# Kernel tuning notes

Measured on AMD Instinct MI355X. Metric: run time of the kernel, lower is better.

## Reference

```python
import jax, jax.numpy as jnp
import numpy as np

B, IN_F, K_INT, OUT_F = 256, 512, 75, 64
INIT = 0.05


def setup_inputs() -> dict:
    key = jax.random.key(0)
    k_x, k_t = jax.random.split(key)
    x = jax.random.normal(k_x, (B, IN_F), dtype=jnp.float32)
    T = jax.random.normal(k_t, (IN_F, K_INT, OUT_F), dtype=jnp.float32) * INIT
    return {"x": x, "T": T}


def reference(x, T):
    # M: [B, K, O] = x @ T flattened over (K, O)
    Bn = x.shape[0]
    M = (x @ T.reshape(T.shape[0], -1)).reshape(Bn, T.shape[1], T.shape[2])
    # pairwise L1 distance over K: [B, B, O]
    # (original materializes [B, B, K, O] broadcasted diff; same math)
    M_diff = M[None, :, :, :] - M[:, None, :, :]
    distance = jnp.abs(M_diff).sum(axis=2)           # [B, B, O]
    exp_distance = jnp.exp(-distance)                # [B, B, O]
    minibatch_features = exp_distance.sum(axis=1) - 1.0  # [B, O]; -1 removes self-distance
    return minibatch_features
```

## Files before the change

kernel.cpp:

```cpp
#include <hip/hip_runtime.h>


typedef __attribute__((ext_vector_type(8))) short bf16x8;
typedef __attribute__((ext_vector_type(4))) float f32x4;
typedef unsigned short u16;
typedef unsigned int u32;

__device__ inline u16 f2bf(float f) {
  u32 u = __float_as_uint(f);
  return (u16)((u + 0x7FFFu + ((u >> 16) & 1u)) >> 16);
}

__global__ __launch_bounds__(256) void cvt_x(const float* __restrict__ x,
                                             u16* __restrict__ xb) {
  const int i = blockIdx.x * 256 + threadIdx.x;
  const float4* x4 = reinterpret_cast<const float4*>(x);
  const float4 v0 = x4[i * 2], v1 = x4[i * 2 + 1];
  uint4 o;
  o.x = (u32)f2bf(v0.x) | ((u32)f2bf(v0.y) << 16);
  o.y = (u32)f2bf(v0.z) | ((u32)f2bf(v0.w) << 16);
  o.z = (u32)f2bf(v1.x) | ((u32)f2bf(v1.y) << 16);
  o.w = (u32)f2bf(v1.z) | ((u32)f2bf(v1.w) << 16);
  *reinterpret_cast<uint4*>(xb + i * 8) = o;
}

__global__ __launch_bounds__(256) void cvt_T(const float* __restrict__ T,
                                             u16* __restrict__ Tb) {
  const int f0 = blockIdx.x << 6;
  const int k = blockIdx.y;
  const int tid = threadIdx.x;
  __shared__ float tile[64][65];

  const float4* T4 = reinterpret_cast<const float4*>(T);
  const int r = tid >> 2;
  const int c = tid & 3;
#pragma unroll
  for (int h = 0; h < 4; ++h) {
    const int q = c + (h << 2);
    const float4 v = T4[(f0 + r) * 1200 + k * 16 + q];
    tile[r][(q << 2) + 0] = v.x;
    tile[r][(q << 2) + 1] = v.y;
    tile[r][(q << 2) + 2] = v.z;
    tile[r][(q << 2) + 3] = v.w;
  }
  __syncthreads();

  const int w = tid >> 2;
  u16 us[16];
#pragma unroll
  for (int j = 0; j < 16; ++j) us[j] = f2bf(tile[(c << 4) + j][w]);
  uint4 p0, p1;
  p0.x = (u32)us[0] | ((u32)us[1] << 16);
  p0.y = (u32)us[2] | ((u32)us[3] << 16);
  p0.z = (u32)us[4] | ((u32)us[5] << 16);
  p0.w = (u32)us[6] | ((u32)us[7] << 16);
  p1.x = (u32)us[8] | ((u32)us[9] << 16);
  p1.y = (u32)us[10] | ((u32)us[11] << 16);
  p1.z = (u32)us[12] | ((u32)us[13] << 16);
  p1.w = (u32)us[14] | ((u32)us[15] << 16);
  uint4* dst = reinterpret_cast<uint4*>(Tb + ((k << 6) + w) * 512 + f0 + (c << 4));
  dst[0] = p0;
  dst[1] = p1;
}

__global__ __launch_bounds__(256) void md_gemm_mfma(const u16* __restrict__ Tb,
                                                    const u16* __restrict__ xb,
                                                    float* __restrict__ Mt) {
  const int tid = threadIdx.x;
  const int l = tid & 63, w = tid >> 6;
  const int n0 = (blockIdx.x << 6) + ((w >> 1) << 5);
  const int b0 = (blockIdx.y << 6) + ((w & 1) << 5);
  const int lr = l & 15;
  const int ko = (l >> 4) << 3;

  const u16* pa0 = Tb + (n0 + lr) * 512 + ko;
  const u16* pa1 = pa0 + 16 * 512;
  const u16* pb0 = xb + (b0 + lr) * 512 + ko;
  const u16* pb1 = pb0 + 16 * 512;

  f32x4 d00 = {0.f, 0.f, 0.f, 0.f}, d01 = d00, d10 = d00, d11 = d00;

#pragma unroll 4
  for (int kk = 0; kk < 16; ++kk) {
    const int off = kk << 5;
    const bf16x8 a0 = *reinterpret_cast<const bf16x8*>(pa0 + off);
    const bf16x8 a1 = *reinterpret_cast<const bf16x8*>(pa1 + off);
    const bf16x8 f0 = *reinterpret_cast<const bf16x8*>(pb0 + off);
    const bf16x8 f1 = *reinterpret_cast<const bf16x8*>(pb1 + off);
    d00 = __builtin_amdgcn_mfma_f32_16x16x32_bf16(a0, f0, d00, 0, 0, 0);
    d01 = __builtin_amdgcn_mfma_f32_16x16x32_bf16(a0, f1, d01, 0, 0, 0);
    d10 = __builtin_amdgcn_mfma_f32_16x16x32_bf16(a1, f0, d10, 0, 0, 0);
    d11 = __builtin_amdgcn_mfma_f32_16x16x32_bf16(a1, f1, d11, 0, 0, 0);
  }

#pragma unroll
  for (int r = 0; r < 4; ++r) {
    const int row = ((l >> 4) << 2) + r;
    {
      const int n = n0 + row;
      float* base = Mt + (n & 63) * 19200 + (n >> 6) * 256;
      base[b0 + lr] = d00[r];
      base[b0 + 16 + lr] = d01[r];
    }
    {
      const int n = n0 + 16 + row;
      float* base = Mt + (n & 63) * 19200 + (n >> 6) * 256;
      base[b0 + lr] = d10[r];
      base[b0 + 16 + lr] = d11[r];
    }
  }
}

__global__ __launch_bounds__(256) void md_pair_sym(const float* __restrict__ Mt,
                                                   float* __restrict__ ps) {
  const int bid = blockIdx.x;
  const int o = bid & 63;
  const int tp = bid >> 6;
  const int TI[10] = {0, 0, 0, 0, 1, 1, 1, 2, 2, 3};
  const int TJ[10] = {0, 1, 2, 3, 1, 2, 3, 2, 3, 3};
  const int ti = TI[tp], tj = TJ[tp];
  const int tid = threadIdx.x;
  const bool diag = (ti == tj);

  __shared__ alignas(16) float sm[2 * 75 * 64];
  float4* Mi4 = reinterpret_cast<float4*>(sm);
  float4* Mj4 = diag ? Mi4 : Mi4 + 75 * 16;

  {
    const float4* src = reinterpret_cast<const float4*>(Mt + o * 19200 + ti * 64);
    for (int t = tid; t < 1200; t += 256) {
      const int k = t >> 4, q = t & 15;
      Mi4[k * 16 + q] = src[k * 64 + q];
    }
    if (!diag) {
      const float4* srj = reinterpret_cast<const float4*>(Mt + o * 19200 + tj * 64);
      for (int t = tid; t < 1200; t += 256) {
        const int k = t >> 4, q = t & 15;
        Mj4[k * 16 + q] = srj[k * 64 + q];
      }
    }
  }
  __syncthreads();

  const int io = tid & 15;
  const int js = tid >> 4;

  float d[4][4];
#pragma unroll
  for (int a = 0; a < 4; ++a)
#pragma unroll
    for (int b = 0; b < 4; ++b) d[a][b] = 0.0f;

  for (int k = 0; k < 75; ++k) {
    const float4 vi = Mi4[k * 16 + io];
    const float4 vj = Mj4[k * 16 + js];
    const float via[4] = {vi.x, vi.y, vi.z, vi.w};
    const float vja[4] = {vj.x, vj.y, vj.z, vj.w};
#pragma unroll
    for (int a = 0; a < 4; ++a)
#pragma unroll
      for (int b = 0; b < 4; ++b) d[a][b] += __builtin_fabsf(vja[b] - via[a]);
  }

  float isum[4] = {0.f, 0.f, 0.f, 0.f};
  float jsum[4] = {0.f, 0.f, 0.f, 0.f};
#pragma unroll
  for (int a = 0; a < 4; ++a)
#pragma unroll
    for (int b = 0; b < 4; ++b) {
      const float e = __expf(-d[a][b]);
      isum[a] += e;
      jsum[b] += e;
    }

  __syncthreads();
  float* red = sm;
#pragma unroll
  for (int a = 0; a < 4; ++a) red[((io << 2) + a) * 17 + js] = isum[a];
  __syncthreads();
  if (tid < 64) {
    float s = 0.0f;
#pragma unroll
    for (int c = 0; c < 16; ++c) s += red[tid * 17 + c];
    ps[(((o << 2) + ti) << 2 | tj) * 64 + tid] = s;
  }
  if (!diag) {
    __syncthreads();
#pragma unroll
    for (int b = 0; b < 4; ++b) red[((js << 2) + b) * 17 + io] = jsum[b];
    __syncthreads();
    if (tid < 64) {
      float s = 0.0f;
#pragma unroll
      for (int c = 0; c < 16; ++c) s += red[tid * 17 + c];
      ps[(((o << 2) + tj) << 2 | ti) * 64 + tid] = s;
    }
  }
}

__global__ __launch_bounds__(256) void md_reduce(const float* __restrict__ ps,
                                                 float* __restrict__ out) {
  const int idx = blockIdx.x * 256 + threadIdx.x;
  const int i = idx >> 6, o = idx & 63;
  const int g = i >> 6, il = i & 63;
  float s = 0.0f;
#pragma unroll
  for (int c = 0; c < 4; ++c) s += ps[(((o << 2) + g) << 2 | c) * 64 + il];
  out[i * 64 + o] = s - 1.0f;
}

extern "C" void kernel_launch(void* const* d_in, const int* in_sizes, int n_in,
                              void* d_out, int out_size, void* d_ws, size_t ws_size,
                              hipStream_t stream) {
  const float* x = (const float*)d_in[0];
  const float* T = (const float*)d_in[1];
  float* out = (float*)d_out;

  char* ws = (char*)d_ws;
  float* Mt = (float*)ws;
  u16* Tb = (u16*)(ws + 4915200);
  u16* xb = (u16*)(ws + 9830400);
  float* ps = (float*)(ws + 10092544);

  cvt_x<<<64, 256, 0, stream>>>(x, xb);
  cvt_T<<<dim3(8, 75), 256, 0, stream>>>(T, Tb);
  md_gemm_mfma<<<dim3(75, 4), 256, 0, stream>>>(Tb, xb, Mt);
  md_pair_sym<<<640, 256, 0, stream>>>(Mt, ps);
  md_reduce<<<64, 256, 0, stream>>>(ps, out);
}
```

Baseline: 53.24 us.

## Merge conversion kernels and replace symmetric pair tiles with full 64-row blocks

Folds the x and T bf16 conversion kernels into one launch. Replaces the symmetric 10-tile pair kernel plus separate reduce kernel with a kernel where each block loads all 256 samples for one output feature and computes 64 rows times 256 columns directly. Each thread now holds an 8x8 register tile and reduces with wave shuffles, writing the final output directly. This removes two launches and the partial-sum buffer, but gives up the symmetry saving, so pairwise work roughly doubles, and the 8x8 tile raises register pressure with only 256 blocks.

Measured after the change: 58.39 us. +9.7%, slower.

```diff
diff --git a/kernel.cpp b/kernel.cpp
--- a/kernel.cpp
+++ b/kernel.cpp
@@ -11,24 +11,28 @@
   return (u16)((u + 0x7FFFu + ((u >> 16) & 1u)) >> 16);
 }
 
-__global__ __launch_bounds__(256) void cvt_x(const float* __restrict__ x,
-                                             u16* __restrict__ xb) {
-  const int i = blockIdx.x * 256 + threadIdx.x;
-  const float4* x4 = reinterpret_cast<const float4*>(x);
-  const float4 v0 = x4[i * 2], v1 = x4[i * 2 + 1];
-  uint4 o;
-  o.x = (u32)f2bf(v0.x) | ((u32)f2bf(v0.y) << 16);
-  o.y = (u32)f2bf(v0.z) | ((u32)f2bf(v0.w) << 16);
-  o.z = (u32)f2bf(v1.x) | ((u32)f2bf(v1.y) << 16);
-  o.w = (u32)f2bf(v1.z) | ((u32)f2bf(v1.w) << 16);
-  *reinterpret_cast<uint4*>(xb + i * 8) = o;
-}
-
-__global__ __launch_bounds__(256) void cvt_T(const float* __restrict__ T,
-                                             u16* __restrict__ Tb) {
-  const int f0 = blockIdx.x << 6;
-  const int k = blockIdx.y;
+__global__ __launch_bounds__(256) void cvt_all(const float* __restrict__ x,
+                                               const float* __restrict__ T,
+                                               u16* __restrict__ xb,
+                                               u16* __restrict__ Tb) {
+  const int bid = blockIdx.x;
   const int tid = threadIdx.x;
+
+  if (bid >= 600) {
+    const int i = (bid - 600) * 256 + tid;
+    const float4* x4 = reinterpret_cast<const float4*>(x);
+    const float4 v0 = x4[i * 2], v1 = x4[i * 2 + 1];
+    uint4 o;
+    o.x = (u32)f2bf(v0.x) | ((u32)f2bf(v0.y) << 16);
+    o.y = (u32)f2bf(v0.z) | ((u32)f2bf(v0.w) << 16);
+    o.z = (u32)f2bf(v1.x) | ((u32)f2bf(v1.y) << 16);
+    o.w = (u32)f2bf(v1.z) | ((u32)f2bf(v1.w) << 16);
+    *reinterpret_cast<uint4*>(xb + i * 8) = o;
+    return;
+  }
+
+  const int f0 = (bid & 7) << 6;
+  const int k = bid >> 3;
   __shared__ float tile[64][65];
 
   const float4* T4 = reinterpret_cast<const float4*>(T);
@@ -111,102 +115,73 @@
   }
 }
 
-__global__ __launch_bounds__(256) void md_pair_sym(const float* __restrict__ Mt,
-                                                   float* __restrict__ ps) {
+__global__ __launch_bounds__(256, 1) void md_pair2(const float* __restrict__ Mt,
+                                                   float* __restrict__ out) {
   const int bid = blockIdx.x;
   const int o = bid & 63;
-  const int tp = bid >> 6;
-  const int TI[10] = {0, 0, 0, 0, 1, 1, 1, 2, 2, 3};
-  const int TJ[10] = {0, 1, 2, 3, 1, 2, 3, 2, 3, 3};
-  const int ti = TI[tp], tj = TJ[tp];
+  const int ibase = (bid >> 6) << 6;
   const int tid = threadIdx.x;
-  const bool diag = (ti == tj);
-
-  __shared__ alignas(16) float sm[2 * 75 * 64];
-  float4* Mi4 = reinterpret_cast<float4*>(sm);
-  float4* Mj4 = diag ? Mi4 : Mi4 + 75 * 16;
+
+  __shared__ alignas(16) float Ms[75 * 256];
 
   {
-    const float4* src = reinterpret_cast<const float4*>(Mt + o * 19200 + ti * 64);
-    for (int t = tid; t < 1200; t += 256) {
-      const int k = t >> 4, q = t & 15;
-      Mi4[k * 16 + q] = src[k * 64 + q];
-    }
-    if (!diag) {
-      const float4* srj = reinterpret_cast<const float4*>(Mt + o * 19200 + tj * 64);
-      for (int t = tid; t < 1200; t += 256) {
-        const int k = t >> 4, q = t & 15;
-        Mj4[k * 16 + q] = srj[k * 64 + q];
-      }
-    }
-  }
-  __syncthreads();
-
-  const int io = tid & 15;
-  const int js = tid >> 4;
-
-  float d[4][4];
-#pragma unroll
-  for (int a = 0; a < 4; ++a)
-#pragma unroll
-    for (int b = 0; b < 4; ++b) d[a][b] = 0.0f;
-
+    const float4* src = reinterpret_cast<const float4*>(Mt + o * 19200);
+    float4* dst = reinterpret_cast<float4*>(Ms);
+    for (int t = tid; t < 4800; t += 256) dst[t] = src[t];
+  }
+  __syncthreads();
+
+  const int is = tid & 7;
+  const int js = tid >> 3;
+  const int ifq = ((ibase >> 2) + (is << 1));
+
+  float d[8][8];
+#pragma unroll
+  for (int a = 0; a < 8; ++a)
+#pragma unroll
+    for (int b = 0; b < 8; ++b) d[a][b] = 0.0f;
+
+#pragma unroll 2
   for (int k = 0; k < 75; ++k) {
-    const float4 vi = Mi4[k * 16 + io];
-    const float4 vj = Mj4[k * 16 + js];
-    const float via[4] = {vi.x, vi.y, vi.z, vi.w};
-    const float vja[4] = {vj.x, vj.y, vj.z, vj.w};
-#pragma unroll
-    for (int a = 0; a < 4; ++a)
-#pragma unroll
-      for (int b = 0; b < 4; ++b) d[a][b] += __builtin_fabsf(vja[b] - via[a]);
-  }
-
-  float isum[4] = {0.f, 0.f, 0.f, 0.f};
-  float jsum[4] = {0.f, 0.f, 0.f, 0.f};
-#pragma unroll
-  for (int a = 0; a < 4; ++a)
-#pragma unroll
-    for (int b = 0; b < 4; ++b) {
-      const float e = __expf(-d[a][b]);
-      isum[a] += e;
-      jsum[b] += e;
-    }
-
-  __syncthreads();
-  float* red = sm;
-#pragma unroll
-  for (int a = 0; a < 4; ++a) red[((io << 2) + a) * 17 + js] = isum[a];
+    const float4* row4 = reinterpret_cast<const float4*>(Ms + (k << 8));
+    const float4 vi0 = row4[ifq];
+    const float4 vi1 = row4[ifq + 1];
+    const float4 vj0 = row4[(js << 1)];
+    const float4 vj1 = row4[(js << 1) + 1];
+    const float ia[8] = {vi0.x, vi0.y, vi0.z, vi0.w, vi1.x, vi1.y, vi1.z, vi1.w};
+    const float ja[8] = {vj0.x, vj0.y, vj0.z, vj0.w, vj1.x, vj1.y, vj1.z, vj1.w};
+#pragma unroll
+    for (int a = 0; a < 8; ++a)
+#pragma unroll
+      for (int b = 0; b < 8; ++b) d[a][b] += __builtin_fabsf(ja[b] - ia[a]);
+  }
+
+  float isum[8];
+#pragma unroll
+  for (int a = 0; a < 8; ++a) {
+    float s = 0.0f;
+#pragma unroll
+    for (int b = 0; b < 8; ++b) s += __expf(-d[a][b]);
+    isum[a] = s;
+  }
+
+#pragma unroll
+  for (int m = 8; m <= 32; m <<= 1)
+#pragma unroll
+    for (int a = 0; a < 8; ++a) isum[a] += __shfl_xor(isum[a], m);
+
+  __syncthreads();
+  float* red = Ms;
+  const int wv = tid >> 6;
+  if (((tid >> 3) & 7) == 0) {
+#pragma unroll
+    for (int a = 0; a < 8; ++a) red[wv * 72 + (is << 3) + a] = isum[a];
+  }
   __syncthreads();
   if (tid < 64) {
-    float s = 0.0f;
-#pragma unroll
-    for (int c = 0; c < 16; ++c) s += red[tid * 17 + c];
-    ps[(((o << 2) + ti) << 2 | tj) * 64 + tid] = s;
-  }
-  if (!diag) {
-    __syncthreads();
-#pragma unroll
-    for (int b = 0; b < 4; ++b) red[((js << 2) + b) * 17 + io] = jsum[b];
-    __syncthreads();
-    if (tid < 64) {
-      float s = 0.0f;
-#pragma unroll
-      for (int c = 0; c < 16; ++c) s += red[tid * 17 + c];
-      ps[(((o << 2) + tj) << 2 | ti) * 64 + tid] = s;
-    }
-  }
-}
-
-__global__ __launch_bounds__(256) void md_reduce(const float* __restrict__ ps,
-                                                 float* __restrict__ out) {
-  const int idx = blockIdx.x * 256 + threadIdx.x;
-  const int i = idx >> 6, o = idx & 63;
-  const int g = i >> 6, il = i & 63;
-  float s = 0.0f;
-#pragma unroll
-  for (int c = 0; c < 4; ++c) s += ps[(((o << 2) + g) << 2 | c) * 64 + il];
-  out[i * 64 + o] = s - 1.0f;
+    const float s = red[tid] + red[72 + tid] + red[144 + tid] + red[216 + tid];
+    out[(ibase + tid) * 64 + o] = s - 1.0f;
+  }
 }
 
 extern "C" void kernel_launch(void* const* d_in, const int* in_sizes, int n_in,
@@ -220,11 +195,8 @@
   float* Mt = (float*)ws;
   u16* Tb = (u16*)(ws + 4915200);
   u16* xb = (u16*)(ws + 9830400);
-  float* ps = (float*)(ws + 10092544);
-
-  cvt_x<<<64, 256, 0, stream>>>(x, xb);
-  cvt_T<<<dim3(8, 75), 256, 0, stream>>>(T, Tb);
+
+  cvt_all<<<664, 256, 0, stream>>>(x, T, xb, Tb);
   md_gemm_mfma<<<dim3(75, 4), 256, 0, stream>>>(Tb, xb, Mt);
-  md_pair_sym<<<640, 256, 0, stream>>>(Mt, ps);
-  md_reduce<<<64, 256, 0, stream>>>(ps, out);
-}
+  md_pair2<<<256, 256, 0, stream>>>(Mt, out);
+}
```
